# Kernel optimization log

Measured on AMD Instinct MI355X. Metric: run time of the kernel, lower is better.

The kernel has to match this reference:

```python
import jax, jax.numpy as jnp
import numpy as np

B, n, A = 64, 1024, 32          # graphs, nodes/graph, actions/graph
N = B * n
EH = 2048                        # undirected edges per graph
HID, H = 128, 4
C = HID // H
NF, EF, AD, NI, L = 1, 1, 7, 4, 3
NEG_SLOPE = 0.2


def setup_inputs() -> dict:
    ks = jax.random.split(jax.random.key(0), 16)
    x = jax.random.normal(ks[0], (N, NF), jnp.float32)
    s = jax.random.randint(ks[1], (B, EH), 0, n)
    d = jax.random.randint(ks[2], (B, EH), 0, n)
    off = (jnp.arange(B) * n)[:, None]
    s = (s + off).reshape(-1)
    d = (d + off).reshape(-1)
    # bidirectional edges (unrooted trees): both i->j and j->i
    edge_index = jnp.stack([jnp.concatenate([s, d]), jnp.concatenate([d, s])]).astype(jnp.int32)
    E = edge_index.shape[1]
    edge_attr = jax.random.uniform(ks[3], (E, EF), jnp.float32)
    idx = jax.random.randint(ks[4], (B, A, NI), 0, n).astype(jnp.float32)
    meta = jax.random.normal(ks[5], (B, A, AD - NI), jnp.float32)
    action_tensor = jnp.concatenate([idx, meta], axis=-1)
    batch_idx = jnp.repeat(jnp.arange(B, dtype=jnp.int32), n)
    batch_ptr = jnp.arange(B + 1, dtype=jnp.int32) * n

    def lin(k, i, o):
        return jax.random.normal(k, (i, o), jnp.float32) / np.float32(np.sqrt(i))

    inp = dict(x=x, edge_attr=edge_attr, action_tensor=action_tensor,
               edge_index=edge_index, batch_idx=batch_idx, batch_ptr=batch_ptr)
    inp["Wn"] = lin(ks[6], NF, HID); inp["bn"] = jnp.zeros((HID,), jnp.float32)
    kl = jax.random.split(ks[7], 4 * L)
    inp["gWl"] = jnp.stack([lin(kl[i], HID, HID) for i in range(L)])
    inp["gWr"] = jnp.stack([lin(kl[L + i], HID, HID) for i in range(L)])
    inp["gWe"] = jnp.stack([lin(kl[2 * L + i], EF, HID) for i in range(L)])
    inp["gatt"] = jnp.stack([jax.random.normal(kl[3 * L + i], (H, C), jnp.float32) * 0.1 for i in range(L)])
    inp["gbl"] = jnp.zeros((L, HID), jnp.float32)
    inp["gbr"] = jnp.zeros((L, HID), jnp.float32)
    inp["gb"] = jnp.zeros((L, HID), jnp.float32)
    mlp_in = NI * HID + (AD - NI)
    inp["aW1"] = lin(ks[8], mlp_in, HID); inp["ab1"] = jnp.zeros((HID,), jnp.float32)
    inp["aW2"] = lin(ks[9], HID, HID); inp["ab2"] = jnp.zeros((HID,), jnp.float32)
    inp["qW1"] = lin(ks[10], 4 * HID, HID); inp["qb1"] = jnp.zeros((HID,), jnp.float32)
    inp["qW2"] = lin(ks[11], HID, HID); inp["qb2"] = jnp.zeros((HID,), jnp.float32)
    inp["qW3"] = lin(ks[12], HID, 1); inp["qb3"] = jnp.zeros((1,), jnp.float32)
    return inp


def _gatv2(h, src, dst, ea, Wl, bl, Wr, br, We, att, b):
    # PyG GATv2Conv: e_ij = att . leaky_relu(lin_l(x_j) + lin_r(x_i) + lin_edge(e_ij))
    Nn = h.shape[0]
    xl = (h @ Wl + bl).reshape(Nn, H, C)   # source transform
    xr = (h @ Wr + br).reshape(Nn, H, C)   # target transform
    ee = (ea @ We).reshape(-1, H, C)       # edge transform (no bias in PyG)
    e = jax.nn.leaky_relu(xl[src] + xr[dst] + ee, NEG_SLOPE)   # [E,H,C]
    logits = jnp.einsum('ehc,hc->eh', e, att)
    m = jax.ops.segment_max(logits, dst, num_segments=Nn)       # stable softmax per target node
    ex = jnp.exp(logits - m[dst])
    alpha = ex / jax.ops.segment_sum(ex, dst, num_segments=Nn)[dst]
    msg = (xl[src] * alpha[:, :, None]).reshape(-1, HID)
    return jax.ops.segment_sum(msg, dst, num_segments=Nn) + b


def reference(x, edge_attr, action_tensor, Wn, bn, gWl, gbl, gWr, gbr, gWe, gatt, gb,
              aW1, ab1, aW2, ab2, qW1, qb1, qW2, qb2, qW3, qb3,
              edge_index, batch_idx, batch_ptr):
    Nn = x.shape[0]
    nb = batch_ptr.shape[0] - 1
    # GATv2Conv default add_self_loops=True, fill_value='mean' for edge_attr
    loops = jnp.arange(Nn, dtype=edge_index.dtype)
    src = jnp.concatenate([edge_index[0], loops])
    dst = jnp.concatenate([edge_index[1], loops])
    ea = jnp.concatenate([edge_attr, jnp.broadcast_to(edge_attr.mean(0), (Nn, edge_attr.shape[1]))], 0)
    h = jax.nn.relu(x @ Wn + bn)
    for l in range(L):
        h = jax.nn.relu(_gatv2(h, src, dst, ea, gWl[l], gbl[l], gWr[l], gbr[l], gWe[l], gatt[l], gb[l])) + h
    # sum / mean / max pooling per graph
    sums = jax.ops.segment_sum(h, batch_idx, num_segments=nb)
    cnt = jax.ops.segment_sum(jnp.ones((Nn, 1), h.dtype), batch_idx, num_segments=nb)
    means = sums / cnt
    maxs = jax.ops.segment_max(h, batch_idx, num_segments=nb)
    tree_emb = jnp.concatenate([sums, means, maxs], -1)          # [B, 3*HID]
    # action encoding: gather node embeddings at action node indices (shifted by batch_ptr)
    ni = action_tensor[..., :NI].astype(jnp.int32) + batch_ptr[:-1][:, None, None]
    g = h[ni].reshape(nb, action_tensor.shape[1], NI * HID)
    ai = jnp.concatenate([g, action_tensor[..., NI:]], -1)
    ae = jax.nn.relu(jax.nn.relu(ai @ aW1 + ab1) @ aW2 + ab2)    # [B, A, HID]
    comb = jnp.concatenate([jnp.broadcast_to(tree_emb[:, None, :], (nb, ae.shape[1], 3 * HID)), ae], -1)
    q = jax.nn.relu(comb @ qW1 + qb1)
    q = jax.nn.relu(q @ qW2 + qb2)
    return (q @ qW3 + qb3).squeeze(-1)                            # [B, A]
```

## Files before the change

### kernel.cpp

```cpp
#include <hip/hip_runtime.h>
#include <hip/hip_bf16.h>

#define NNODES 65536
#define NGRAPH 64
#define NPG 1024
#define NACT 32
#define HID 128
#define DEGS 32

typedef __attribute__((ext_vector_type(8))) short bf16x8;
typedef __attribute__((ext_vector_type(4))) float f32x4;

__device__ __forceinline__ void load8(float* dst, const float* src) {
    float4 q0 = ((const float4*)src)[0];
    float4 q1 = ((const float4*)src)[1];
    dst[0]=q0.x; dst[1]=q0.y; dst[2]=q0.z; dst[3]=q0.w;
    dst[4]=q1.x; dst[5]=q1.y; dst[6]=q1.z; dst[7]=q1.w;
}

__device__ __forceinline__ void load8bf(float* dst, const unsigned short* src) {
    uint4 q = *(const uint4*)src;
    unsigned int u0 = q.x, u1 = q.y, u2 = q.z, u3 = q.w;
    dst[0] = __uint_as_float(u0 << 16); dst[1] = __uint_as_float(u0 & 0xffff0000u);
    dst[2] = __uint_as_float(u1 << 16); dst[3] = __uint_as_float(u1 & 0xffff0000u);
    dst[4] = __uint_as_float(u2 << 16); dst[5] = __uint_as_float(u2 & 0xffff0000u);
    dst[6] = __uint_as_float(u3 << 16); dst[7] = __uint_as_float(u3 & 0xffff0000u);
}

__device__ __forceinline__ unsigned short f2bf(float f) {
    unsigned int u = __float_as_uint(f);
    u = (u + 0x7fffu + ((u >> 16) & 1u)) >> 16;
    return (unsigned short)u;
}

__global__ void setup_k(const int* __restrict__ ei, const float* __restrict__ ea,
                        int* __restrict__ cursor, float* __restrict__ meansum,
                        int2* __restrict__ csr, int E0, int nsb,
                        const float* __restrict__ gWl, const float* __restrict__ gWr,
                        unsigned short* __restrict__ wtl, unsigned short* __restrict__ wtr,
                        const float* __restrict__ aW1, const float* __restrict__ aW2,
                        const float* __restrict__ qW1, const float* __restrict__ qW2,
                        unsigned short* __restrict__ wA1t, unsigned short* __restrict__ wA2t,
                        unsigned short* __restrict__ wQ1t, unsigned short* __restrict__ wQ2t) {
    int bid = blockIdx.x, t = threadIdx.x;
    if (bid < nsb) {
        __shared__ float s[256];
        int e = bid * 256 + t;
        float v = 0.f;
        if (e < E0) {
            int sn = ei[e], d = ei[E0 + e];
            int pos = atomicAdd(&cursor[d], 1);
            if (pos >= DEGS) pos = DEGS - 1;
            csr[(size_t)d * DEGS + pos] = make_int2(sn, __float_as_int(ea[e]));
            v = ea[e];
        }
        s[t] = v; __syncthreads();
        for (int off = 128; off > 0; off >>= 1) { if (t < off) s[t] += s[t+off]; __syncthreads(); }
        if (t == 0) atomicAdd(meansum, s[0]);
    } else if (bid < nsb + 192) {
        int idx = (bid - nsb) * 256 + t;
        int l = idx >> 14, rem = idx & 16383;
        int n = rem >> 7, k = rem & 127;
        int src = l*16384 + k*128 + n;
        wtl[idx] = f2bf(gWl[src]);
        wtr[idx] = f2bf(gWr[src]);
    } else {
        int n = bid - nsb - 192;
        for (int k = t; k < 544; k += 256)
            wA1t[n*544 + k] = (k < 515) ? f2bf(aW1[(size_t)k*128 + n]) : (unsigned short)0;
        if (t < 128) {
            wA2t[n*128 + t] = f2bf(aW2[(size_t)t*128 + n]);
            wQ1t[n*128 + t] = f2bf(qW1[(size_t)(384 + t)*128 + n]);
            wQ2t[n*128 + t] = f2bf(qW2[(size_t)t*128 + n]);
        }
    }
}

__global__ __launch_bounds__(256) void gemm_lr_mfma_k(
    const unsigned short* __restrict__ hb, const float* __restrict__ x,
    const float* __restrict__ Wn, const float* __restrict__ bn, int l0,
    const unsigned short* __restrict__ wtl, const unsigned short* __restrict__ wtr,
    const float* __restrict__ bl, const float* __restrict__ br,
    unsigned short* __restrict__ xlb, unsigned short* __restrict__ xrb) {
    int wave = threadIdx.x >> 6;
    int lane = threadIdx.x & 63;
    int lr = lane & 15;
    int lq = lane >> 4;
    int r0 = blockIdx.x * 128 + wave * 32;

    bf16x8 a[2][4];
    if (l0) {
        float xv0 = x[r0 + lr], xv1 = x[r0 + 16 + lr];
#pragma unroll
        for (int kf = 0; kf < 4; ++kf) {
            float wn[8], bv[8];
            load8(wn, Wn + kf*32 + lq*8);
            load8(bv, bn + kf*32 + lq*8);
            union { bf16x8 v; unsigned short u[8]; } p0, p1;
#pragma unroll
            for (int j = 0; j < 8; ++j) {
                p0.u[j] = f2bf(fmaxf(fmaf(xv0, wn[j], bv[j]), 0.f));
                p1.u[j] = f2bf(fmaxf(fmaf(xv1, wn[j], bv[j]), 0.f));
            }
            a[0][kf] = p0.v; a[1][kf] = p1.v;
        }
    } else {
        const short* hs = (const short*)hb;
#pragma unroll
        for (int rt = 0; rt < 2; ++rt)
#pragma unroll
            for (int kf = 0; kf < 4; ++kf)
                a[rt][kf] = *(const bf16x8*)(hs + (size_t)(r0 + rt*16 + lr)*HID + kf*32 + lq*8);
    }

    const short* ws[2]   = {(const short*)wtl, (const short*)wtr};
    const float* bias[2] = {bl, br};
    unsigned short* outp[2] = {xlb, xrb};

#pragma unroll
    for (int m = 0; m < 2; ++m) {
        const short* W = ws[m];
        f32x4 acc[2][8];
#pragma unroll
        for (int rt = 0; rt < 2; ++rt)
#pragma unroll
            for (int ct = 0; ct < 8; ++ct) acc[rt][ct] = (f32x4){0.f,0.f,0.f,0.f};

        bf16x8 b[4], nb[4];
#pragma unroll
        for (int kf = 0; kf < 4; ++kf)
            b[kf] = *(const bf16x8*)(W + (size_t)(lr)*HID + kf*32 + lq*8);
#pragma unroll
        for (int ct = 0; ct < 8; ++ct) {
            if (ct < 7) {
#pragma unroll
                for (int kf = 0; kf < 4; ++kf)
                    nb[kf] = *(const bf16x8*)(W + (size_t)((ct+1)*16 + lr)*HID + kf*32 + lq*8);
            }
#pragma unroll
            for (int rt = 0; rt < 2; ++rt)
#pragma unroll
                for (int kf = 0; kf < 4; ++kf)
                    acc[rt][ct] = __builtin_amdgcn_mfma_f32_16x16x32_bf16(a[rt][kf], b[kf], acc[rt][ct], 0, 0, 0);
#pragma unroll
            for (int kf = 0; kf < 4; ++kf) b[kf] = nb[kf];
        }
#pragma unroll
        for (int ct = 0; ct < 8; ++ct) {
            float bv = bias[m][ct*16 + lr];
#pragma unroll
            for (int rt = 0; rt < 2; ++rt)
#pragma unroll
                for (int rg = 0; rg < 4; ++rg) {
                    int row = r0 + rt*16 + lq*4 + rg;
                    outp[m][(size_t)row*HID + ct*16 + lr] = f2bf(acc[rt][ct][rg] + bv);
                }
        }
    }
}

__global__ __launch_bounds__(256, 4) void gat_edge_k(
    const unsigned short* __restrict__ xlb, const unsigned short* __restrict__ xrb,
    unsigned short* __restrict__ hb,
    const int* __restrict__ deg, const int2* __restrict__ csr,
    const float* __restrict__ We, const float* __restrict__ att,
    const float* __restrict__ gb, const float* __restrict__ meansum, float inv_e0,
    const float* __restrict__ x, const float* __restrict__ Wn, const float* __restrict__ bn,
    int l0, int do_pool, float* __restrict__ tree_sum, float* __restrict__ tree_max) {
    __shared__ float ps[16][132];
    __shared__ float pm[16][132];
    int xcd  = blockIdx.x & 7;
    int slot = blockIdx.x >> 3;
    int g    = xcd * 8 + (slot >> 6);
    int j    = slot & 63;
    int t    = threadIdx.x;
    int nd   = t >> 4;
    int v    = g * NPG + j * 16 + nd;
    int li   = t & 15;
    int base = li * 8;
    float mea = meansum[0] * inv_e0;

    float xrv[8], attv[8], wev[8];
    load8bf(xrv, xrb + (size_t)v*HID + base);
    load8(attv, att + base);
    load8(wev, We + base);

    float acc[8], xA[8];
    load8bf(xA, xlb + (size_t)v*HID + base);
    float m;
    {
        float lg = 0.f;
#pragma unroll
        for (int c = 0; c < 8; ++c) {
            float e = xA[c] + xrv[c] + mea * wev[c];
            e = fmaxf(e, 0.2f * e);
            lg = fmaf(attv[c], e, lg);
        }
        lg += __shfl_xor(lg, 1, 64);
        lg += __shfl_xor(lg, 2, 64);
        m = lg;
#pragma unroll
        for (int c = 0; c < 8; ++c) acc[c] = xA[c];
    }
    float den = 1.f;

    int dg = deg[v];
    if (dg > DEGS) dg = DEGS;
    if (dg > 0) {
        const int2* cp = csr + (size_t)v * DEGS;
        int2 e0 = cp[0];
        int2 e1 = cp[(1 < dg) ? 1 : dg - 1];
        float xB[8];
        load8bf(xA, xlb + (size_t)e0.x*HID + base);
        load8bf(xB, xlb + (size_t)e1.x*HID + base);
        for (int i = 0; i < dg; ++i) {
            int2 e2 = cp[(i + 2 < dg) ? i + 2 : dg - 1];
            float xC[8];
            load8bf(xC, xlb + (size_t)e2.x*HID + base);
            float an = __int_as_float(e0.y);

            float lg = 0.f;
#pragma unroll
            for (int c = 0; c < 8; ++c) {
                float e = xA[c] + xrv[c] + an * wev[c];
                e = fmaxf(e, 0.2f * e);
                lg = fmaf(attv[c], e, lg);
            }
            lg += __shfl_xor(lg, 1, 64);
            lg += __shfl_xor(lg, 2, 64);

            float mn  = fmaxf(m, lg);
            float sc  = __expf(m - mn);
            float wgt = __expf(lg - mn);
            den = den * sc + wgt;
#pragma unroll
            for (int c = 0; c < 8; ++c) acc[c] = acc[c] * sc + wgt * xA[c];
            m = mn;
            e0 = e1; e1 = e2;
#pragma unroll
            for (int c = 0; c < 8; ++c) { xA[c] = xB[c]; xB[c] = xC[c]; }
        }
    }

    float inv = 1.f / den;
    size_t o = (size_t)v*HID + base;
    float hold[8], gbv[8];
    if (l0) {
        float xv = x[v];
        float wn[8], bv[8];
        load8(wn, Wn + base);
        load8(bv, bn + base);
#pragma unroll
        for (int c = 0; c < 8; ++c) hold[c] = fmaxf(fmaf(xv, wn[c], bv[c]), 0.f);
    } else {
        load8bf(hold, hb + o);
    }
    load8(gbv, gb + base);
    float nh[8];
#pragma unroll
    for (int c = 0; c < 8; ++c) {
        float val = acc[c] * inv + gbv[c];
        val = val > 0.f ? val : 0.f;
        nh[c] = val + hold[c];
    }
    unsigned int* hbp = (unsigned int*)(hb + o);
#pragma unroll
    for (int q = 0; q < 4; ++q)
        hbp[q] = (unsigned int)f2bf(nh[2*q]) | ((unsigned int)f2bf(nh[2*q+1]) << 16);

    if (do_pool) {
#pragma unroll
        for (int c = 0; c < 8; ++c) { ps[nd][base + c] = nh[c]; pm[nd][base + c] = nh[c]; }
        __syncthreads();
        if (t < 128) {
            float s = 0.f;
#pragma unroll
            for (int n = 0; n < 16; ++n) s += ps[n][t];
            atomicAdd(&tree_sum[g*128 + t], s);
        } else {
            int col = t - 128;
            float mx = 0.f;
#pragma unroll
            for (int n = 0; n < 16; ++n) mx = fmaxf(mx, pm[n][col]);
            atomicMax((int*)&tree_max[g*128 + col], __float_as_int(mx));
        }
    }
}

#define SA1 552
#define SAC 136
__global__ __launch_bounds__(256) void action_q_k(
    const unsigned short* __restrict__ hb, const float* __restrict__ action,
    const int* __restrict__ batch_ptr,
    const float* __restrict__ tree_sum, const float* __restrict__ tree_max,
    const unsigned short* __restrict__ wA1t, const float* __restrict__ ab1,
    const unsigned short* __restrict__ wA2t, const float* __restrict__ ab2,
    const float* __restrict__ qW1, const unsigned short* __restrict__ wQ1t,
    const float* __restrict__ qb1,
    const unsigned short* __restrict__ wQ2t, const float* __restrict__ qb2,
    const float* __restrict__ qW3, const float* __restrict__ qb3,
    float* __restrict__ out) {
    int b = blockIdx.x;
    int t = threadIdx.x;
    int w  = t >> 6;
    int lane = t & 63;
    int lr = lane & 15;
    int lq = lane >> 4;

    __shared__ unsigned short aib[32 * SA1];
    __shared__ unsigned short z1s[32 * SAC];
    __shared__ unsigned short aes[32 * SAC];
    __shared__ unsigned short q1s[32 * SAC];
    __shared__ float q2f[32 * 132];
    __shared__ float tqA[128], tqB[128];
    __shared__ float psum[32][8];

    int ptr = batch_ptr[b];

    {
        int p = t >> 1, half = t & 1;
        int a = p >> 2, j = p & 3;
        const float* actp = action + (size_t)(b * NACT + a) * 7;
        int ni = (int)actp[j] + ptr;
        const uint4* src = (const uint4*)(hb + (size_t)ni * HID) + half * 8;
        uint4* dst = (uint4*)((char*)aib + ((size_t)a * SA1 + j * 128 + half * 64) * 2);
#pragma unroll
        for (int q = 0; q < 8; ++q) dst[q] = src[q];
        if (t < 32) {
            const float* ap = action + (size_t)(b * NACT + t) * 7;
            aib[t * SA1 + 512] = f2bf(ap[4]);
            aib[t * SA1 + 513] = f2bf(ap[5]);
            aib[t * SA1 + 514] = f2bf(ap[6]);
            for (int i = 3; i < 40; ++i) aib[t * SA1 + 512 + i] = 0;
        }
    }

    {
        if (t < 128) {
            int col = t;
            float acc = 0.f;
#pragma unroll 4
            for (int k = 0; k < 128; ++k) {
                float sv = tree_sum[b * 128 + k];
                acc = fmaf(sv, qW1[(size_t)k * 128 + col], acc);
                acc = fmaf(sv * (1.f / 1024.f), qW1[(size_t)(128 + k) * 128 + col], acc);
            }
            tqA[col] = acc;
        } else {
            int col = t - 128;
            float acc = 0.f;
#pragma unroll 4
            for (int k = 0; k < 128; ++k) {
                float mv = tree_max[b * 128 + k];
                acc = fmaf(mv, qW1[(size_t)(256 + k) * 128 + col], acc);
            }
            tqB[col] = acc;
        }
    }
    __syncthreads();

    f32x4 acc[2][2];
    const unsigned short* srcA;
    int strideA, K;

    srcA = aib; strideA = SA1; K = 544;
#pragma unroll
    for (int rt = 0; rt < 2; ++rt)
#pragma unroll
        for (int ci = 0; ci < 2; ++ci) acc[rt][ci] = (f32x4){0.f, 0.f, 0.f, 0.f};
    for (int ks = 0; ks < K; ks += 32) {
        bf16x8 a0 = *(const bf16x8*)(srcA + (0 * 16 + lr) * strideA + ks + lq * 8);
        bf16x8 a1 = *(const bf16x8*)(srcA + (1 * 16 + lr) * strideA + ks + lq * 8);
        bf16x8 b0 = *(const bf16x8*)(wA1t + (size_t)((2 * w + 0) * 16 + lr) * K + ks + lq * 8);
        bf16x8 b1 = *(const bf16x8*)(wA1t + (size_t)((2 * w + 1) * 16 + lr) * K + ks + lq * 8);
        acc[0][0] = __builtin_amdgcn_mfma_f32_16x16x32_bf16(a0, b0, acc[0][0], 0, 0, 0);
        acc[0][1] = __builtin_amdgcn_mfma_f32_16x16x32_bf16(a0, b1, acc[0][1], 0, 0, 0);
        acc[1][0] = __builtin_amdgcn_mfma_f32_16x16x32_bf16(a1, b0, acc[1][0], 0, 0, 0);
        acc[1][1] = __builtin_amdgcn_mfma_f32_16x16x32_bf16(a1, b1, acc[1][1], 0, 0, 0);
    }
#pragma unroll
    for (int ci = 0; ci < 2; ++ci) {
        int col = (2 * w + ci) * 16 + lr;
        float bv = ab1[col];
#pragma unroll
        for (int rt = 0; rt < 2; ++rt)
#pragma unroll
            for (int rg = 0; rg < 4; ++rg) {
                int row = rt * 16 + lq * 4 + rg;
                z1s[row * SAC + col] = f2bf(fmaxf(acc[rt][ci][rg] + bv, 0.f));
            }
    }
    __syncthreads();

    srcA = z1s; strideA = SAC; K = 128;
#pragma unroll
    for (int rt = 0; rt < 2; ++rt)
#pragma unroll
        for (int ci = 0; ci < 2; ++ci) acc[rt][ci] = (f32x4){0.f, 0.f, 0.f, 0.f};
#pragma unroll
    for (int ks = 0; ks < 128; ks += 32) {
        bf16x8 a0 = *(const bf16x8*)(srcA + (0 * 16 + lr) * strideA + ks + lq * 8);
        bf16x8 a1 = *(const bf16x8*)(srcA + (1 * 16 + lr) * strideA + ks + lq * 8);
        bf16x8 b0 = *(const bf16x8*)(wA2t + (size_t)((2 * w + 0) * 16 + lr) * K + ks + lq * 8);
        bf16x8 b1 = *(const bf16x8*)(wA2t + (size_t)((2 * w + 1) * 16 + lr) * K + ks + lq * 8);
        acc[0][0] = __builtin_amdgcn_mfma_f32_16x16x32_bf16(a0, b0, acc[0][0], 0, 0, 0);
        acc[0][1] = __builtin_amdgcn_mfma_f32_16x16x32_bf16(a0, b1, acc[0][1], 0, 0, 0);
        acc[1][0] = __builtin_amdgcn_mfma_f32_16x16x32_bf16(a1, b0, acc[1][0], 0, 0, 0);
        acc[1][1] = __builtin_amdgcn_mfma_f32_16x16x32_bf16(a1, b1, acc[1][1], 0, 0, 0);
    }
#pragma unroll
    for (int ci = 0; ci < 2; ++ci) {
        int col = (2 * w + ci) * 16 + lr;
        float bv = ab2[col];
#pragma unroll
        for (int rt = 0; rt < 2; ++rt)
#pragma unroll
            for (int rg = 0; rg < 4; ++rg) {
                int row = rt * 16 + lq * 4 + rg;
                aes[row * SAC + col] = f2bf(fmaxf(acc[rt][ci][rg] + bv, 0.f));
            }
    }
    __syncthreads();

    srcA = aes; strideA = SAC; K = 128;
#pragma unroll
    for (int rt = 0; rt < 2; ++rt)
#pragma unroll
        for (int ci = 0; ci < 2; ++ci) acc[rt][ci] = (f32x4){0.f, 0.f, 0.f, 0.f};
#pragma unroll
    for (int ks = 0; ks < 128; ks += 32) {
        bf16x8 a0 = *(const bf16x8*)(srcA + (0 * 16 + lr) * strideA + ks + lq * 8);
        bf16x8 a1 = *(const bf16x8*)(srcA + (1 * 16 + lr) * strideA + ks + lq * 8);
        bf16x8 b0 = *(const bf16x8*)(wQ1t + (size_t)((2 * w + 0) * 16 + lr) * K + ks + lq * 8);
        bf16x8 b1 = *(const bf16x8*)(wQ1t + (size_t)((2 * w + 1) * 16 + lr) * K + ks + lq * 8);
        acc[0][0] = __builtin_amdgcn_mfma_f32_16x16x32_bf16(a0, b0, acc[0][0], 0, 0, 0);
        acc[0][1] = __builtin_amdgcn_mfma_f32_16x16x32_bf16(a0, b1, acc[0][1], 0, 0, 0);
        acc[1][0] = __builtin_amdgcn_mfma_f32_16x16x32_bf16(a1, b0, acc[1][0], 0, 0, 0);
        acc[1][1] = __builtin_amdgcn_mfma_f32_16x16x32_bf16(a1, b1, acc[1][1], 0, 0, 0);
    }
#pragma unroll
    for (int ci = 0; ci < 2; ++ci) {
        int col = (2 * w + ci) * 16 + lr;
        float bv = qb1[col] + tqA[col] + tqB[col];
#pragma unroll
        for (int rt = 0; rt < 2; ++rt)
#pragma unroll
            for (int rg = 0; rg < 4; ++rg) {
                int row = rt * 16 + lq * 4 + rg;
                q1s[row * SAC + col] = f2bf(fmaxf(acc[rt][ci][rg] + bv, 0.f));
            }
    }
    __syncthreads();

    srcA = q1s; strideA = SAC; K = 128;
#pragma unroll
    for (int rt = 0; rt < 2; ++rt)
#pragma unroll
        for (int ci = 0; ci < 2; ++ci) acc[rt][ci] = (f32x4){0.f, 0.f, 0.f, 0.f};
#pragma unroll
    for (int ks = 0; ks < 128; ks += 32) {
        bf16x8 a0 = *(const bf16x8*)(srcA + (0 * 16 + lr) * strideA + ks + lq * 8);
        bf16x8 a1 = *(const bf16x8*)(srcA + (1 * 16 + lr) * strideA + ks + lq * 8);
        bf16x8 b0 = *(const bf16x8*)(wQ2t + (size_t)((2 * w + 0) * 16 + lr) * K + ks + lq * 8);
        bf16x8 b1 = *(const bf16x8*)(wQ2t + (size_t)((2 * w + 1) * 16 + lr) * K + ks + lq * 8);
        acc[0][0] = __builtin_amdgcn_mfma_f32_16x16x32_bf16(a0, b0, acc[0][0], 0, 0, 0);
        acc[0][1] = __builtin_amdgcn_mfma_f32_16x16x32_bf16(a0, b1, acc[0][1], 0, 0, 0);
        acc[1][0] = __builtin_amdgcn_mfma_f32_16x16x32_bf16(a1, b0, acc[1][0], 0, 0, 0);
        acc[1][1] = __builtin_amdgcn_mfma_f32_16x16x32_bf16(a1, b1, acc[1][1], 0, 0, 0);
    }
#pragma unroll
    for (int ci = 0; ci < 2; ++ci) {
        int col = (2 * w + ci) * 16 + lr;
        float bv = qb2[col];
#pragma unroll
        for (int rt = 0; rt < 2; ++rt)
#pragma unroll
            for (int rg = 0; rg < 4; ++rg) {
                int row = rt * 16 + lq * 4 + rg;
                q2f[row * 132 + col] = fmaxf(acc[rt][ci][rg] + bv, 0.f);
            }
    }
    __syncthreads();

    {
        int a = t >> 3, seg = t & 7;
        float s = 0.f;
#pragma unroll
        for (int k = 0; k < 16; ++k)
            s = fmaf(q2f[a * 132 + seg * 16 + k], qW3[seg * 16 + k], s);
        psum[a][seg] = s;
    }
    __syncthreads();
    if (t < 32) {
        float s = qb3[0];
#pragma unroll
        for (int i = 0; i < 8; ++i) s += psum[t][i];
        out[(size_t)b * NACT + t] = s;
    }
}

extern "C" void kernel_launch(void* const* d_in, const int* in_sizes, int n_in,
                              void* d_out, int out_size, void* d_ws, size_t ws_size,
                              hipStream_t stream) {
    const float* x         = (const float*)d_in[0];
    const float* edge_attr = (const float*)d_in[1];
    const float* action    = (const float*)d_in[2];
    const int*   edge_idx  = (const int*)d_in[3];
    const int*   batch_ptr = (const int*)d_in[5];
    const float* Wn  = (const float*)d_in[6];
    const float* bn  = (const float*)d_in[7];
    const float* gWl = (const float*)d_in[8];
    const float* gWr = (const float*)d_in[9];
    const float* gWe = (const float*)d_in[10];
    const float* gatt= (const float*)d_in[11];
    const float* gbl = (const float*)d_in[12];
    const float* gbr = (const float*)d_in[13];
    const float* gb  = (const float*)d_in[14];
    const float* aW1 = (const float*)d_in[15];
    const float* ab1 = (const float*)d_in[16];
    const float* aW2 = (const float*)d_in[17];
    const float* ab2 = (const float*)d_in[18];
    const float* qW1 = (const float*)d_in[19];
    const float* qb1 = (const float*)d_in[20];
    const float* qW2 = (const float*)d_in[21];
    const float* qb2 = (const float*)d_in[22];
    const float* qW3 = (const float*)d_in[23];
    const float* qb3 = (const float*)d_in[24];
    float* out = (float*)d_out;

    const int E0 = in_sizes[1];
    const int N  = NNODES;

    char* w = (char*)d_ws;
    auto alloc = [&](size_t bytes) { void* p = (void*)w; w += (bytes + 255) & ~(size_t)255; return p; };
    unsigned short* hb  = (unsigned short*)alloc((size_t)N * HID * 2);
    unsigned short* xlb = (unsigned short*)alloc((size_t)N * HID * 2);
    unsigned short* xrb = (unsigned short*)alloc((size_t)N * HID * 2);
    int2*  csr      = (int2*)alloc((size_t)N * DEGS * 8);
    int*   cursor   = (int*)alloc((size_t)N * 4);
    float* meansum  = (float*)alloc(256);
    float* tree_sum = (float*)alloc((size_t)NGRAPH * 128 * 4);
    float* tree_max = (float*)alloc((size_t)NGRAPH * 128 * 4);
    size_t zero_span = (size_t)((char*)(tree_max + NGRAPH * 128) - (char*)cursor);
    unsigned short* wtl = (unsigned short*)alloc((size_t)3*128*128*2);
    unsigned short* wtr = (unsigned short*)alloc((size_t)3*128*128*2);
    unsigned short* wA1t = (unsigned short*)alloc((size_t)128*544*2);
    unsigned short* wA2t = (unsigned short*)alloc((size_t)128*128*2);
    unsigned short* wQ1t = (unsigned short*)alloc((size_t)128*128*2);
    unsigned short* wQ2t = (unsigned short*)alloc((size_t)128*128*2);

    hipMemsetAsync(cursor, 0, zero_span, stream);

    int nsb = (E0 + 255) / 256;
    setup_k<<<nsb + 320, 256, 0, stream>>>(edge_idx, edge_attr, cursor, meansum, csr, E0, nsb,
                                           gWl, gWr, wtl, wtr,
                                           aW1, aW2, qW1, qW2, wA1t, wA2t, wQ1t, wQ2t);

    float inv_e0 = 1.0f / (float)E0;
    for (int l = 0; l < 3; ++l) {
        gemm_lr_mfma_k<<<N / 128, 256, 0, stream>>>(
            hb, x, Wn, bn, (l == 0) ? 1 : 0,
            wtl + (size_t)l*128*128, wtr + (size_t)l*128*128,
            gbl + l*HID, gbr + l*HID, xlb, xrb);
        gat_edge_k<<<N / 16, 256, 0, stream>>>(
            xlb, xrb, hb, cursor, csr,
            gWe + l*HID, gatt + l*128, gb + l*HID, meansum, inv_e0,
            x, Wn, bn, (l == 0) ? 1 : 0, (l == 2) ? 1 : 0, tree_sum, tree_max);
    }

    action_q_k<<<NGRAPH, 256, 0, stream>>>(
        hb, action, batch_ptr, tree_sum, tree_max,
        wA1t, ab1, wA2t, ab2, qW1, wQ1t, qb1, wQ2t, qb2, qW3, qb3, out);
}
```

Before: 310.3 us.

## Fuse next-layer GEMM into GAT aggregation and fold action head into final layer

Each GAT aggregation kernel now stages its 16 new node rows in shared memory and immediately computes the next layer's left/right projections with MFMA. This removes the separate per-layer GEMM launches and the extra read of h. The final layer pools per graph and uses a per-graph completion counter, so the last block for each graph runs the action/Q MLP head, which removes a separate kernel launch. The xl/xr buffers are double-buffered because the next layer's outputs are written while neighbours still read the current ones. The trade-off is that each block reloads weight tiles from global or L2, and the last block per graph must wait on atomics plus a fence.

```diff
diff --git a/kernel.cpp b/kernel.cpp
--- a/kernel.cpp
+++ b/kernel.cpp
@@ -7,6 +7,7 @@
 #define NACT 32
 #define HID 128
 #define DEGS 32
+#define SAC 136
 
 typedef __attribute__((ext_vector_type(8))) short bf16x8;
 typedef __attribute__((ext_vector_type(4))) float f32x4;
@@ -17,16 +18,13 @@
     dst[0]=q0.x; dst[1]=q0.y; dst[2]=q0.z; dst[3]=q0.w;
     dst[4]=q1.x; dst[5]=q1.y; dst[6]=q1.z; dst[7]=q1.w;
 }
-
 __device__ __forceinline__ void load8bf(float* dst, const unsigned short* src) {
     uint4 q = *(const uint4*)src;
-    unsigned int u0 = q.x, u1 = q.y, u2 = q.z, u3 = q.w;
-    dst[0] = __uint_as_float(u0 << 16); dst[1] = __uint_as_float(u0 & 0xffff0000u);
-    dst[2] = __uint_as_float(u1 << 16); dst[3] = __uint_as_float(u1 & 0xffff0000u);
-    dst[4] = __uint_as_float(u2 << 16); dst[5] = __uint_as_float(u2 & 0xffff0000u);
-    dst[6] = __uint_as_float(u3 << 16); dst[7] = __uint_as_float(u3 & 0xffff0000u);
-}
-
+    dst[0] = __uint_as_float(q.x << 16); dst[1] = __uint_as_float(q.x & 0xffff0000u);
+    dst[2] = __uint_as_float(q.y << 16); dst[3] = __uint_as_float(q.y & 0xffff0000u);
+    dst[4] = __uint_as_float(q.z << 16); dst[5] = __uint_as_float(q.z & 0xffff0000u);
+    dst[6] = __uint_as_float(q.w << 16); dst[7] = __uint_as_float(q.w & 0xffff0000u);
+}
 __device__ __forceinline__ unsigned short f2bf(float f) {
     unsigned int u = __float_as_uint(f);
     u = (u + 0x7fffu + ((u >> 16) & 1u)) >> 16;
@@ -76,47 +74,34 @@
     }
 }
 
-__global__ __launch_bounds__(256) void gemm_lr_mfma_k(
-    const unsigned short* __restrict__ hb, const float* __restrict__ x,
-    const float* __restrict__ Wn, const float* __restrict__ bn, int l0,
+__global__ __launch_bounds__(256) void gemm0_k(
+    const float* __restrict__ x, const float* __restrict__ Wn, const float* __restrict__ bn,
     const unsigned short* __restrict__ wtl, const unsigned short* __restrict__ wtr,
     const float* __restrict__ bl, const float* __restrict__ br,
     unsigned short* __restrict__ xlb, unsigned short* __restrict__ xrb) {
-    int wave = threadIdx.x >> 6;
-    int lane = threadIdx.x & 63;
-    int lr = lane & 15;
-    int lq = lane >> 4;
+    int wave = threadIdx.x >> 6, lane = threadIdx.x & 63;
+    int lr = lane & 15, lq = lane >> 4;
     int r0 = blockIdx.x * 128 + wave * 32;
 
     bf16x8 a[2][4];
-    if (l0) {
-        float xv0 = x[r0 + lr], xv1 = x[r0 + 16 + lr];
-#pragma unroll
-        for (int kf = 0; kf < 4; ++kf) {
-            float wn[8], bv[8];
-            load8(wn, Wn + kf*32 + lq*8);
-            load8(bv, bn + kf*32 + lq*8);
-            union { bf16x8 v; unsigned short u[8]; } p0, p1;
-#pragma unroll
-            for (int j = 0; j < 8; ++j) {
-                p0.u[j] = f2bf(fmaxf(fmaf(xv0, wn[j], bv[j]), 0.f));
-                p1.u[j] = f2bf(fmaxf(fmaf(xv1, wn[j], bv[j]), 0.f));
-            }
-            a[0][kf] = p0.v; a[1][kf] = p1.v;
-        }
-    } else {
-        const short* hs = (const short*)hb;
-#pragma unroll
-        for (int rt = 0; rt < 2; ++rt)
-#pragma unroll
-            for (int kf = 0; kf < 4; ++kf)
-                a[rt][kf] = *(const bf16x8*)(hs + (size_t)(r0 + rt*16 + lr)*HID + kf*32 + lq*8);
+    float xv0 = x[r0 + lr], xv1 = x[r0 + 16 + lr];
+#pragma unroll
+    for (int kf = 0; kf < 4; ++kf) {
+        float wn[8], bv[8];
+        load8(wn, Wn + kf*32 + lq*8);
+        load8(bv, bn + kf*32 + lq*8);
+        union { bf16x8 v; unsigned short u[8]; } p0, p1;
+#pragma unroll
+        for (int j = 0; j < 8; ++j) {
+            p0.u[j] = f2bf(fmaxf(fmaf(xv0, wn[j], bv[j]), 0.f));
+            p1.u[j] = f2bf(fmaxf(fmaf(xv1, wn[j], bv[j]), 0.f));
+        }
+        a[0][kf] = p0.v; a[1][kf] = p1.v;
     }
 
     const short* ws[2]   = {(const short*)wtl, (const short*)wtr};
     const float* bias[2] = {bl, br};
     unsigned short* outp[2] = {xlb, xrb};
-
 #pragma unroll
     for (int m = 0; m < 2; ++m) {
         const short* W = ws[m];
@@ -125,17 +110,16 @@
         for (int rt = 0; rt < 2; ++rt)
 #pragma unroll
             for (int ct = 0; ct < 8; ++ct) acc[rt][ct] = (f32x4){0.f,0.f,0.f,0.f};
-
-        bf16x8 b[4], nb[4];
+        bf16x8 b[4], nb2[4];
 #pragma unroll
         for (int kf = 0; kf < 4; ++kf)
-            b[kf] = *(const bf16x8*)(W + (size_t)(lr)*HID + kf*32 + lq*8);
+            b[kf] = *(const bf16x8*)(W + (size_t)lr*HID + kf*32 + lq*8);
 #pragma unroll
         for (int ct = 0; ct < 8; ++ct) {
             if (ct < 7) {
 #pragma unroll
                 for (int kf = 0; kf < 4; ++kf)
-                    nb[kf] = *(const bf16x8*)(W + (size_t)((ct+1)*16 + lr)*HID + kf*32 + lq*8);
+                    nb2[kf] = *(const bf16x8*)(W + (size_t)((ct+1)*16 + lr)*HID + kf*32 + lq*8);
             }
 #pragma unroll
             for (int rt = 0; rt < 2; ++rt)
@@ -143,7 +127,7 @@
                 for (int kf = 0; kf < 4; ++kf)
                     acc[rt][ct] = __builtin_amdgcn_mfma_f32_16x16x32_bf16(a[rt][kf], b[kf], acc[rt][ct], 0, 0, 0);
 #pragma unroll
-            for (int kf = 0; kf < 4; ++kf) b[kf] = nb[kf];
+            for (int kf = 0; kf < 4; ++kf) b[kf] = nb2[kf];
         }
 #pragma unroll
         for (int ct = 0; ct < 8; ++ct) {
@@ -151,24 +135,190 @@
 #pragma unroll
             for (int rt = 0; rt < 2; ++rt)
 #pragma unroll
-                for (int rg = 0; rg < 4; ++rg) {
-                    int row = r0 + rt*16 + lq*4 + rg;
-                    outp[m][(size_t)row*HID + ct*16 + lr] = f2bf(acc[rt][ct][rg] + bv);
-                }
-        }
-    }
-}
-
-__global__ __launch_bounds__(256, 4) void gat_edge_k(
-    const unsigned short* __restrict__ xlb, const unsigned short* __restrict__ xrb,
+                for (int rg = 0; rg < 4; ++rg)
+                    outp[m][(size_t)(r0 + rt*16 + lq*4 + rg)*HID + ct*16 + lr] = f2bf(acc[rt][ct][rg] + bv);
+        }
+    }
+}
+
+
+__global__ __launch_bounds__(256, 4) void gatgemm_k(
+    const unsigned short* __restrict__ xli, const unsigned short* __restrict__ xri,
     unsigned short* __restrict__ hb,
     const int* __restrict__ deg, const int2* __restrict__ csr,
     const float* __restrict__ We, const float* __restrict__ att,
     const float* __restrict__ gb, const float* __restrict__ meansum, float inv_e0,
-    const float* __restrict__ x, const float* __restrict__ Wn, const float* __restrict__ bn,
-    int l0, int do_pool, float* __restrict__ tree_sum, float* __restrict__ tree_max) {
-    __shared__ float ps[16][132];
-    __shared__ float pm[16][132];
+    const float* __restrict__ x, const float* __restrict__ Wn, const float* __restrict__ bn, int l0,
+    const unsigned short* __restrict__ wtlN, const unsigned short* __restrict__ wtrN,
+    const float* __restrict__ blN, const float* __restrict__ brN,
+    unsigned short* __restrict__ xlo, unsigned short* __restrict__ xro) {
+    __shared__ unsigned short sA[16 * SAC];
+    int xcd  = blockIdx.x & 7;
+    int slot = blockIdx.x >> 3;
+    int g    = xcd * 8 + (slot >> 6);
+    int j    = slot & 63;
+    int t    = threadIdx.x;
+    int nd   = t >> 4;
+    int vb   = g * NPG + j * 16;
+    int v    = vb + nd;
+    int li   = t & 15;
+    int base = li * 8;
+    float mea = meansum[0] * inv_e0;
+
+    float xrv[8], attv[8], wev[8];
+    load8bf(xrv, xri + (size_t)v*HID + base);
+    load8(attv, att + base);
+    load8(wev, We + base);
+
+    float acc[8], xA[8];
+    load8bf(xA, xli + (size_t)v*HID + base);
+    float m;
+    {
+        float lg = 0.f;
+#pragma unroll
+        for (int c = 0; c < 8; ++c) {
+            float e = xA[c] + xrv[c] + mea * wev[c];
+            e = fmaxf(e, 0.2f * e);
+            lg = fmaf(attv[c], e, lg);
+        }
+        lg += __shfl_xor(lg, 1, 64);
+        lg += __shfl_xor(lg, 2, 64);
+        m = lg;
+#pragma unroll
+        for (int c = 0; c < 8; ++c) acc[c] = xA[c];
+    }
+    float den = 1.f;
+
+    int dg = deg[v];
+    if (dg > DEGS) dg = DEGS;
+    if (dg > 0) {
+        const int2* cp = csr + (size_t)v * DEGS;
+        int2 e0 = cp[0];
+        int2 e1 = cp[(1 < dg) ? 1 : dg - 1];
+        float xB[8];
+        load8bf(xA, xli + (size_t)e0.x*HID + base);
+        load8bf(xB, xli + (size_t)e1.x*HID + base);
+        for (int i = 0; i < dg; ++i) {
+            int2 e2 = cp[(i + 2 < dg) ? i + 2 : dg - 1];
+            float xC[8];
+            load8bf(xC, xli + (size_t)e2.x*HID + base);
+            float an = __int_as_float(e0.y);
+            float lg = 0.f;
+#pragma unroll
+            for (int c = 0; c < 8; ++c) {
+                float e = xA[c] + xrv[c] + an * wev[c];
+                e = fmaxf(e, 0.2f * e);
+                lg = fmaf(attv[c], e, lg);
+            }
+            lg += __shfl_xor(lg, 1, 64);
+            lg += __shfl_xor(lg, 2, 64);
+            float mn  = fmaxf(m, lg);
+            float sc  = __expf(m - mn);
+            float wgt = __expf(lg - mn);
+            den = den * sc + wgt;
+#pragma unroll
+            for (int c = 0; c < 8; ++c) acc[c] = acc[c] * sc + wgt * xA[c];
+            m = mn;
+            e0 = e1; e1 = e2;
+#pragma unroll
+            for (int c = 0; c < 8; ++c) { xA[c] = xB[c]; xB[c] = xC[c]; }
+        }
+    }
+
+    float inv = 1.f / den;
+    size_t o = (size_t)v*HID + base;
+    float hold[8], gbv[8];
+    if (l0) {
+        float xv = x[v];
+        float wn[8], bv[8];
+        load8(wn, Wn + base);
+        load8(bv, bn + base);
+#pragma unroll
+        for (int c = 0; c < 8; ++c) hold[c] = fmaxf(fmaf(xv, wn[c], bv[c]), 0.f);
+    } else {
+        load8bf(hold, hb + o);
+    }
+    load8(gbv, gb + base);
+    float nh[8];
+#pragma unroll
+    for (int c = 0; c < 8; ++c) {
+        float val = acc[c] * inv + gbv[c];
+        val = val > 0.f ? val : 0.f;
+        nh[c] = val + hold[c];
+    }
+    unsigned int pk[4];
+#pragma unroll
+    for (int q = 0; q < 4; ++q)
+        pk[q] = (unsigned int)f2bf(nh[2*q]) | ((unsigned int)f2bf(nh[2*q+1]) << 16);
+    unsigned int* hbp = (unsigned int*)(hb + o);
+#pragma unroll
+    for (int q = 0; q < 4; ++q) hbp[q] = pk[q];
+    unsigned int* sAp = (unsigned int*)(sA + nd * SAC + base);
+#pragma unroll
+    for (int q = 0; q < 4; ++q) sAp[q] = pk[q];
+    __syncthreads();
+
+    int wave = t >> 6, lane = t & 63, lr = lane & 15, lq = lane >> 4;
+    bf16x8 afr[4];
+#pragma unroll
+    for (int kf = 0; kf < 4; ++kf)
+        afr[kf] = *(const bf16x8*)(sA + lr * SAC + kf*32 + lq*8);
+    const short* ws[2]   = {(const short*)wtlN, (const short*)wtrN};
+    const float* bias[2] = {blN, brN};
+    unsigned short* outp[2] = {xlo, xro};
+#pragma unroll
+    for (int mm = 0; mm < 2; ++mm) {
+        const short* W = ws[mm];
+        f32x4 gac[2];
+#pragma unroll
+        for (int ci = 0; ci < 2; ++ci) gac[ci] = (f32x4){0.f,0.f,0.f,0.f};
+#pragma unroll
+        for (int ci = 0; ci < 2; ++ci) {
+            int ct = wave * 2 + ci;
+#pragma unroll
+            for (int kf = 0; kf < 4; ++kf) {
+                bf16x8 bv = *(const bf16x8*)(W + (size_t)(ct*16 + lr)*HID + kf*32 + lq*8);
+                gac[ci] = __builtin_amdgcn_mfma_f32_16x16x32_bf16(afr[kf], bv, gac[ci], 0, 0, 0);
+            }
+        }
+#pragma unroll
+        for (int ci = 0; ci < 2; ++ci) {
+            int ct = wave * 2 + ci;
+            float bv = bias[mm][ct*16 + lr];
+#pragma unroll
+            for (int rg = 0; rg < 4; ++rg)
+                outp[mm][(size_t)(vb + lq*4 + rg)*HID + ct*16 + lr] = f2bf(gac[ci][rg] + bv);
+        }
+    }
+}
+
+__global__ __launch_bounds__(256, 4) void gatfinal_k(
+    const unsigned short* __restrict__ xli, const unsigned short* __restrict__ xri,
+    unsigned short* __restrict__ hb,
+    const int* __restrict__ deg, const int2* __restrict__ csr,
+    const float* __restrict__ We, const float* __restrict__ att,
+    const float* __restrict__ gb, const float* __restrict__ meansum, float inv_e0,
+    float* __restrict__ tree_s, float* __restrict__ tree_m, int* __restrict__ done,
+    const float* __restrict__ action, const int* __restrict__ batch_ptr,
+    const unsigned short* __restrict__ wA1t, const float* __restrict__ ab1,
+    const unsigned short* __restrict__ wA2t, const float* __restrict__ ab2,
+    const float* __restrict__ qW1, const unsigned short* __restrict__ wQ1t,
+    const float* __restrict__ qb1,
+    const unsigned short* __restrict__ wQ2t, const float* __restrict__ qb2,
+    const float* __restrict__ qW3, const float* __restrict__ qb3,
+    float* __restrict__ out) {
+    __shared__ __align__(16) char arena[38912];
+    float* pool = (float*)arena;
+    int*            s_ni = (int*)arena;
+    unsigned short* amt  = (unsigned short*)(arena + 512);
+    float*          tqA  = (float*)(arena + 2560);
+    float*          tqB  = (float*)(arena + 3072);
+    float*          psum = (float*)(arena + 3584);
+    unsigned short* z1s  = (unsigned short*)(arena + 4608);
+    unsigned short* aes  = (unsigned short*)(arena + 13312);
+    float*          q2f  = (float*)(arena + 22016);
+    __shared__ int lastflag;
+
     int xcd  = blockIdx.x & 7;
     int slot = blockIdx.x >> 3;
     int g    = xcd * 8 + (slot >> 6);
@@ -181,12 +331,12 @@
     float mea = meansum[0] * inv_e0;
 
     float xrv[8], attv[8], wev[8];
-    load8bf(xrv, xrb + (size_t)v*HID + base);
+    load8bf(xrv, xri + (size_t)v*HID + base);
     load8(attv, att + base);
     load8(wev, We + base);
 
     float acc[8], xA[8];
-    load8bf(xA, xlb + (size_t)v*HID + base);
+    load8bf(xA, xli + (size_t)v*HID + base);
     float m;
     {
         float lg = 0.f;
@@ -211,14 +361,13 @@
         int2 e0 = cp[0];
         int2 e1 = cp[(1 < dg) ? 1 : dg - 1];
         float xB[8];
-        load8bf(xA, xlb + (size_t)e0.x*HID + base);
-        load8bf(xB, xlb + (size_t)e1.x*HID + base);
+        load8bf(xA, xli + (size_t)e0.x*HID + base);
+        load8bf(xB, xli + (size_t)e1.x*HID + base);
         for (int i = 0; i < dg; ++i) {
             int2 e2 = cp[(i + 2 < dg) ? i + 2 : dg - 1];
             float xC[8];
-            load8bf(xC, xlb + (size_t)e2.x*HID + base);
+            load8bf(xC, xli + (size_t)e2.x*HID + base);
             float an = __int_as_float(e0.y);
-
             float lg = 0.f;
 #pragma unroll
             for (int c = 0; c < 8; ++c) {
@@ -228,7 +377,6 @@
             }
             lg += __shfl_xor(lg, 1, 64);
             lg += __shfl_xor(lg, 2, 64);
-
             float mn  = fmaxf(m, lg);
             float sc  = __expf(m - mn);
             float wgt = __expf(lg - mn);
@@ -245,16 +393,7 @@
     float inv = 1.f / den;
     size_t o = (size_t)v*HID + base;
     float hold[8], gbv[8];
-    if (l0) {
-        float xv = x[v];
-        float wn[8], bv[8];
-        load8(wn, Wn + base);
-        load8(bv, bn + base);
-#pragma unroll
-        for (int c = 0; c < 8; ++c) hold[c] = fmaxf(fmaf(xv, wn[c], bv[c]), 0.f);
-    } else {
-        load8bf(hold, hb + o);
-    }
+    load8bf(hold, hb + o);
     load8(gbv, gb + base);
     float nh[8];
 #pragma unroll
@@ -268,234 +407,198 @@
     for (int q = 0; q < 4; ++q)
         hbp[q] = (unsigned int)f2bf(nh[2*q]) | ((unsigned int)f2bf(nh[2*q+1]) << 16);
 
-    if (do_pool) {
-#pragma unroll
-        for (int c = 0; c < 8; ++c) { ps[nd][base + c] = nh[c]; pm[nd][base + c] = nh[c]; }
-        __syncthreads();
-        if (t < 128) {
-            float s = 0.f;
-#pragma unroll
-            for (int n = 0; n < 16; ++n) s += ps[n][t];
-            atomicAdd(&tree_sum[g*128 + t], s);
+#pragma unroll
+    for (int c = 0; c < 8; ++c) {
+        pool[nd*132 + base + c]        = nh[c];
+        pool[2112 + nd*132 + base + c] = nh[c];
+    }
+    __syncthreads();
+    if (t < 128) {
+        float s = 0.f;
+#pragma unroll
+        for (int n = 0; n < 16; ++n) s += pool[n*132 + t];
+        atomicAdd(&tree_s[g*128 + t], s);
+    } else {
+        int col = t - 128;
+        float mx = 0.f;
+#pragma unroll
+        for (int n = 0; n < 16; ++n) mx = fmaxf(mx, pool[2112 + n*132 + col]);
+        atomicMax((int*)&tree_m[g*128 + col], __float_as_int(mx));
+    }
+    __syncthreads();
+
+    if (t == 0) {
+        __threadfence();
+        int old = atomicAdd(&done[g], 1);
+        lastflag = (old == 63);
+    }
+    __syncthreads();
+    if (!lastflag) return;
+    __threadfence();
+
+    int wave = t >> 6, lane = t & 63, lr = lane & 15, lq = lane >> 4;
+    int ptr = batch_ptr[g];
+    if (t < 128) {
+        int a = t >> 2, jj = t & 3;
+        s_ni[t] = (int)action[(size_t)(g*NACT + a)*7 + jj] + ptr;
+    } else if (t < 160) {
+        int a = t - 128;
+        const float* ap = action + (size_t)(g*NACT + a)*7;
+        amt[a*32 + 0] = f2bf(ap[4]);
+        amt[a*32 + 1] = f2bf(ap[5]);
+        amt[a*32 + 2] = f2bf(ap[6]);
+        for (int i = 3; i < 32; ++i) amt[a*32 + i] = 0;
+    }
+    __syncthreads();
+    if (t < 128) {
+        int col = t;
+        float a2 = 0.f;
+#pragma unroll 4
+        for (int k = 0; k < 128; ++k) {
+            float sv = tree_s[g*128 + k];
+            a2 = fmaf(sv, qW1[(size_t)k*128 + col], a2);
+            a2 = fmaf(sv * (1.f/1024.f), qW1[(size_t)(128 + k)*128 + col], a2);
+        }
+        tqA[col] = a2;
+    } else {
+        int col = t - 128;
+        float a2 = 0.f;
+#pragma unroll 4
+        for (int k = 0; k < 128; ++k)
+            a2 = fmaf(tree_m[g*128 + k], qW1[(size_t)(256 + k)*128 + col], a2);
+        tqB[col] = a2;
+    }
+    __syncthreads();
+
+    const short* hbs = (const short*)hb;
+    f32x4 qac[2][2];
+#pragma unroll
+    for (int rt = 0; rt < 2; ++rt)
+#pragma unroll
+        for (int ci = 0; ci < 2; ++ci) qac[rt][ci] = (f32x4){0.f,0.f,0.f,0.f};
+    for (int ks = 0; ks < 544; ks += 32) {
+        bf16x8 a0, a1;
+        if (ks < 512) {
+            int n0 = s_ni[(0*16 + lr)*4 + (ks >> 7)];
+            int n1 = s_ni[(1*16 + lr)*4 + (ks >> 7)];
+            a0 = *(const bf16x8*)(hbs + (size_t)n0*HID + (ks & 127) + lq*8);
+            a1 = *(const bf16x8*)(hbs + (size_t)n1*HID + (ks & 127) + lq*8);
         } else {
-            int col = t - 128;
-            float mx = 0.f;
-#pragma unroll
-            for (int n = 0; n < 16; ++n) mx = fmaxf(mx, pm[n][col]);
-            atomicMax((int*)&tree_max[g*128 + col], __float_as_int(mx));
-        }
-    }
-}
-
-#define SA1 552
-#define SAC 136
-__global__ __launch_bounds__(256) void action_q_k(
-    const unsigned short* __restrict__ hb, const float* __restrict__ action,
-    const int* __restrict__ batch_ptr,
-    const float* __restrict__ tree_sum, const float* __restrict__ tree_max,
-    const unsigned short* __restrict__ wA1t, const float* __restrict__ ab1,
-    const unsigned short* __restrict__ wA2t, const float* __restrict__ ab2,
-    const float* __restrict__ qW1, const unsigned short* __restrict__ wQ1t,
-    const float* __restrict__ qb1,
-    const unsigned short* __restrict__ wQ2t, const float* __restrict__ qb2,
-    const float* __restrict__ qW3, const float* __restrict__ qb3,
-    float* __restrict__ out) {
-    int b = blockIdx.x;
-    int t = threadIdx.x;
-    int w  = t >> 6;
-    int lane = t & 63;
-    int lr = lane & 15;
-    int lq = lane >> 4;
-
-    __shared__ unsigned short aib[32 * SA1];
-    __shared__ unsigned short z1s[32 * SAC];
-    __shared__ unsigned short aes[32 * SAC];
-    __shared__ unsigned short q1s[32 * SAC];
-    __shared__ float q2f[32 * 132];
-    __shared__ float tqA[128], tqB[128];
-    __shared__ float psum[32][8];
-
-    int ptr = batch_ptr[b];
-
-    {
-        int p = t >> 1, half = t & 1;
-        int a = p >> 2, j = p & 3;
-        const float* actp = action + (size_t)(b * NACT + a) * 7;
-        int ni = (int)actp[j] + ptr;
-        const uint4* src = (const uint4*)(hb + (size_t)ni * HID) + half * 8;
-        uint4* dst = (uint4*)((char*)aib + ((size_t)a * SA1 + j * 128 + half * 64) * 2);
-#pragma unroll
-        for (int q = 0; q < 8; ++q) dst[q] = src[q];
-        if (t < 32) {
-            const float* ap = action + (size_t)(b * NACT + t) * 7;
-            aib[t * SA1 + 512] = f2bf(ap[4]);
-            aib[t * SA1 + 513] = f2bf(ap[5]);
-            aib[t * SA1 + 514] = f2bf(ap[6]);
-            for (int i = 3; i < 40; ++i) aib[t * SA1 + 512 + i] = 0;
-        }
-    }
-
-    {
-        if (t < 128) {
-            int col = t;
-            float acc = 0.f;
-#pragma unroll 4
-            for (int k = 0; k < 128; ++k) {
-                float sv = tree_sum[b * 128 + k];
-                acc = fmaf(sv, qW1[(size_t)k * 128 + col], acc);
-                acc = fmaf(sv * (1.f / 1024.f), qW1[(size_t)(128 + k) * 128 + col], acc);
-            }
-            tqA[col] = acc;
-        } else {
-            int col = t - 128;
-            float acc = 0.f;
-#pragma unroll 4
-            for (int k = 0; k < 128; ++k) {
-                float mv = tree_max[b * 128 + k];
-                acc = fmaf(mv, qW1[(size_t)(256 + k) * 128 + col], acc);
-            }
-            tqB[col] = acc;
-        }
-    }
-    __syncthreads();
-
-    f32x4 acc[2][2];
-    const unsigned short* srcA;
-    int strideA, K;
-
-    srcA = aib; strideA = SA1; K = 544;
+            a0 = *(const bf16x8*)(amt + (0*16 + lr)*32 + lq*8);
+            a1 = *(const bf16x8*)(amt + (1*16 + lr)*32 + lq*8);
+        }
+        bf16x8 b0 = *(const bf16x8*)(wA1t + (size_t)((2*wave+0)*16 + lr)*544 + ks + lq*8);
+        bf16x8 b1 = *(const bf16x8*)(wA1t + (size_t)((2*wave+1)*16 + lr)*544 + ks + lq*8);
+        qac[0][0] = __builtin_amdgcn_mfma_f32_16x16x32_bf16(a0, b0, qac[0][0], 0, 0, 0);
+        qac[0][1] = __builtin_amdgcn_mfma_f32_16x16x32_bf16(a0, b1, qac[0][1], 0, 0, 0);
+        qac[1][0] = __builtin_amdgcn_mfma_f32_16x16x32_bf16(a1, b0, qac[1][0], 0, 0, 0);
+        qac[1][1] = __builtin_amdgcn_mfma_f32_16x16x32_bf16(a1, b1, qac[1][1], 0, 0, 0);
+    }
+#pragma unroll
+    for (int ci = 0; ci < 2; ++ci) {
+        int col = (2*wave + ci)*16 + lr;
+        float bv = ab1[col];
+#pragma unroll
+        for (int rt = 0; rt < 2; ++rt)
+#pragma unroll
+            for (int rg = 0; rg < 4; ++rg)
+                z1s[(rt*16 + lq*4 + rg)*SAC + col] = f2bf(fmaxf(qac[rt][ci][rg] + bv, 0.f));
+    }
+    __syncthreads();
 #pragma unroll
     for (int rt = 0; rt < 2; ++rt)
 #pragma unroll
-        for (int ci = 0; ci < 2; ++ci) acc[rt][ci] = (f32x4){0.f, 0.f, 0.f, 0.f};
-    for (int ks = 0; ks < K; ks += 32) {
-        bf16x8 a0 = *(const bf16x8*)(srcA + (0 * 16 + lr) * strideA + ks + lq * 8);
-        bf16x8 a1 = *(const bf16x8*)(srcA + (1 * 16 + lr) * strideA + ks + lq * 8);
-        bf16x8 b0 = *(const bf16x8*)(wA1t + (size_t)((2 * w + 0) * 16 + lr) * K + ks + lq * 8);
-        bf16x8 b1 = *(const bf16x8*)(wA1t + (size_t)((2 * w + 1) * 16 + lr) * K + ks + lq * 8);
-        acc[0][0] = __builtin_amdgcn_mfma_f32_16x16x32_bf16(a0, b0, acc[0][0], 0, 0, 0);
-        acc[0][1] = __builtin_amdgcn_mfma_f32_16x16x32_bf16(a0, b1, acc[0][1], 0, 0, 0);
-        acc[1][0] = __builtin_amdgcn_mfma_f32_16x16x32_bf16(a1, b0, acc[1][0], 0, 0, 0);
-        acc[1][1] = __builtin_amdgcn_mfma_f32_16x16x32_bf16(a1, b1, acc[1][1], 0, 0, 0);
-    }
+        for (int ci = 0; ci < 2; ++ci) qac[rt][ci] = (f32x4){0.f,0.f,0.f,0.f};
+#pragma unroll
+    for (int ks = 0; ks < 128; ks += 32) {
+        bf16x8 a0 = *(const bf16x8*)(z1s + (0*16 + lr)*SAC + ks + lq*8);
+        bf16x8 a1 = *(const bf16x8*)(z1s + (1*16 + lr)*SAC + ks + lq*8);
+        bf16x8 b0 = *(const bf16x8*)(wA2t + (size_t)((2*wave+0)*16 + lr)*128 + ks + lq*8);
+        bf16x8 b1 = *(const bf16x8*)(wA2t + (size_t)((2*wave+1)*16 + lr)*128 + ks + lq*8);
+        qac[0][0] = __builtin_amdgcn_mfma_f32_16x16x32_bf16(a0, b0, qac[0][0], 0, 0, 0);
+        qac[0][1] = __builtin_amdgcn_mfma_f32_16x16x32_bf16(a0, b1, qac[0][1], 0, 0, 0);
+        qac[1][0] = __builtin_amdgcn_mfma_f32_16x16x32_bf16(a1, b0, qac[1][0], 0, 0, 0);
+        qac[1][1] = __builtin_amdgcn_mfma_f32_16x16x32_bf16(a1, b1, qac[1][1], 0, 0, 0);
+    }
+    __syncthreads();
 #pragma unroll
     for (int ci = 0; ci < 2; ++ci) {
-        int col = (2 * w + ci) * 16 + lr;
-        float bv = ab1[col];
+        int col = (2*wave + ci)*16 + lr;
+        float bv = ab2[col];
 #pragma unroll
         for (int rt = 0; rt < 2; ++rt)
 #pragma unroll
-            for (int rg = 0; rg < 4; ++rg) {
-                int row = rt * 16 + lq * 4 + rg;
-                z1s[row * SAC + col] = f2bf(fmaxf(acc[rt][ci][rg] + bv, 0.f));
-            }
-    }
-    __syncthreads();
-
-    srcA = z1s; strideA = SAC; K = 128;
+            for (int rg = 0; rg < 4; ++rg)
+                aes[(rt*16 + lq*4 + rg)*SAC + col] = f2bf(fmaxf(qac[rt][ci][rg] + bv, 0.f));
+    }
+    __syncthreads();
 #pragma unroll
     for (int rt = 0; rt < 2; ++rt)
 #pragma unroll
-        for (int ci = 0; ci < 2; ++ci) acc[rt][ci] = (f32x4){0.f, 0.f, 0.f, 0.f};
+        for (int ci = 0; ci < 2; ++ci) qac[rt][ci] = (f32x4){0.f,0.f,0.f,0.f};
 #pragma unroll
     for (int ks = 0; ks < 128; ks += 32) {
-        bf16x8 a0 = *(const bf16x8*)(srcA + (0 * 16 + lr) * strideA + ks + lq * 8);
-        bf16x8 a1 = *(const bf16x8*)(srcA + (1 * 16 + lr) * strideA + ks + lq * 8);
-        bf16x8 b0 = *(const bf16x8*)(wA2t + (size_t)((2 * w + 0) * 16 + lr) * K + ks + lq * 8);
-        bf16x8 b1 = *(const bf16x8*)(wA2t + (size_t)((2 * w + 1) * 16 + lr) * K + ks + lq * 8);
-        acc[0][0] = __builtin_amdgcn_mfma_f32_16x16x32_bf16(a0, b0, acc[0][0], 0, 0, 0);
-        acc[0][1] = __builtin_amdgcn_mfma_f32_16x16x32_bf16(a0, b1, acc[0][1], 0, 0, 0);
-        acc[1][0] = __builtin_amdgcn_mfma_f32_16x16x32_bf16(a1, b0, acc[1][0], 0, 0, 0);
-        acc[1][1] = __builtin_amdgcn_mfma_f32_16x16x32_bf16(a1, b1, acc[1][1], 0, 0, 0);
-    }
+        bf16x8 a0 = *(const bf16x8*)(aes + (0*16 + lr)*SAC + ks + lq*8);
+        bf16x8 a1 = *(const bf16x8*)(aes + (1*16 + lr)*SAC + ks + lq*8);
+        bf16x8 b0 = *(const bf16x8*)(wQ1t + (size_t)((2*wave+0)*16 + lr)*128 + ks + lq*8);
+        bf16x8 b1 = *(const bf16x8*)(wQ1t + (size_t)((2*wave+1)*16 + lr)*128 + ks + lq*8);
+        qac[0][0] = __builtin_amdgcn_mfma_f32_16x16x32_bf16(a0, b0, qac[0][0], 0, 0, 0);
+        qac[0][1] = __builtin_amdgcn_mfma_f32_16x16x32_bf16(a0, b1, qac[0][1], 0, 0, 0);
+        qac[1][0] = __builtin_amdgcn_mfma_f32_16x16x32_bf16(a1, b0, qac[1][0], 0, 0, 0);
+        qac[1][1] = __builtin_amdgcn_mfma_f32_16x16x32_bf16(a1, b1, qac[1][1], 0, 0, 0);
+    }
+    __syncthreads();
 #pragma unroll
     for (int ci = 0; ci < 2; ++ci) {
-        int col = (2 * w + ci) * 16 + lr;
-        float bv = ab2[col];
+        int col = (2*wave + ci)*16 + lr;
+        float bv = qb1[col] + tqA[col] + tqB[col];
 #pragma unroll
         for (int rt = 0; rt < 2; ++rt)
 #pragma unroll
-            for (int rg = 0; rg < 4; ++rg) {
-                int row = rt * 16 + lq * 4 + rg;
-                aes[row * SAC + col] = f2bf(fmaxf(acc[rt][ci][rg] + bv, 0.f));
-            }
-    }
-    __syncthreads();
-
-    srcA = aes; strideA = SAC; K = 128;
+            for (int rg = 0; rg < 4; ++rg)
+                z1s[(rt*16 + lq*4 + rg)*SAC + col] = f2bf(fmaxf(qac[rt][ci][rg] + bv, 0.f));
+    }
+    __syncthreads();
 #pragma unroll
     for (int rt = 0; rt < 2; ++rt)
 #pragma unroll
-        for (int ci = 0; ci < 2; ++ci) acc[rt][ci] = (f32x4){0.f, 0.f, 0.f, 0.f};
+        for (int ci = 0; ci < 2; ++ci) qac[rt][ci] = (f32x4){0.f,0.f,0.f,0.f};
 #pragma unroll
     for (int ks = 0; ks < 128; ks += 32) {
-        bf16x8 a0 = *(const bf16x8*)(srcA + (0 * 16 + lr) * strideA + ks + lq * 8);
-        bf16x8 a1 = *(const bf16x8*)(srcA + (1 * 16 + lr) * strideA + ks + lq * 8);
-        bf16x8 b0 = *(const bf16x8*)(wQ1t + (size_t)((2 * w + 0) * 16 + lr) * K + ks + lq * 8);
-        bf16x8 b1 = *(const bf16x8*)(wQ1t + (size_t)((2 * w + 1) * 16 + lr) * K + ks + lq * 8);
-        acc[0][0] = __builtin_amdgcn_mfma_f32_16x16x32_bf16(a0, b0, acc[0][0], 0, 0, 0);
-        acc[0][1] = __builtin_amdgcn_mfma_f32_16x16x32_bf16(a0, b1, acc[0][1], 0, 0, 0);
-        acc[1][0] = __builtin_amdgcn_mfma_f32_16x16x32_bf16(a1, b0, acc[1][0], 0, 0, 0);
-        acc[1][1] = __builtin_amdgcn_mfma_f32_16x16x32_bf16(a1, b1, acc[1][1], 0, 0, 0);
+        bf16x8 a0 = *(const bf16x8*)(z1s + (0*16 + lr)*SAC + ks + lq*8);
+        bf16x8 a1 = *(const bf16x8*)(z1s + (1*16 + lr)*SAC + ks + lq*8);
+        bf16x8 b0 = *(const bf16x8*)(wQ2t + (size_t)((2*wave+0)*16 + lr)*128 + ks + lq*8);
+        bf16x8 b1 = *(const bf16x8*)(wQ2t + (size_t)((2*wave+1)*16 + lr)*128 + ks + lq*8);
+        qac[0][0] = __builtin_amdgcn_mfma_f32_16x16x32_bf16(a0, b0, qac[0][0], 0, 0, 0);
+        qac[0][1] = __builtin_amdgcn_mfma_f32_16x16x32_bf16(a0, b1, qac[0][1], 0, 0, 0);
+        qac[1][0] = __builtin_amdgcn_mfma_f32_16x16x32_bf16(a1, b0, qac[1][0], 0, 0, 0);
+        qac[1][1] = __builtin_amdgcn_mfma_f32_16x16x32_bf16(a1, b1, qac[1][1], 0, 0, 0);
     }
 #pragma unroll
     for (int ci = 0; ci < 2; ++ci) {
-        int col = (2 * w + ci) * 16 + lr;
-        float bv = qb1[col] + tqA[col] + tqB[col];
+        int col = (2*wave + ci)*16 + lr;
+        float bv = qb2[col];
 #pragma unroll
         for (int rt = 0; rt < 2; ++rt)
 #pragma unroll
-            for (int rg = 0; rg < 4; ++rg) {
-                int row = rt * 16 + lq * 4 + rg;
-                q1s[row * SAC + col] = f2bf(fmaxf(acc[rt][ci][rg] + bv, 0.f));
-            }
-    }
-    __syncthreads();
-
-    srcA = q1s; strideA = SAC; K = 128;
-#pragma unroll
-    for (int rt = 0; rt < 2; ++rt)
-#pragma unroll
-        for (int ci = 0; ci < 2; ++ci) acc[rt][ci] = (f32x4){0.f, 0.f, 0.f, 0.f};
-#pragma unroll
-    for (int ks = 0; ks < 128; ks += 32) {
-        bf16x8 a0 = *(const bf16x8*)(srcA + (0 * 16 + lr) * strideA + ks + lq * 8);
-        bf16x8 a1 = *(const bf16x8*)(srcA + (1 * 16 + lr) * strideA + ks + lq * 8);
-        bf16x8 b0 = *(const bf16x8*)(wQ2t + (size_t)((2 * w + 0) * 16 + lr) * K + ks + lq * 8);
-        bf16x8 b1 = *(const bf16x8*)(wQ2t + (size_t)((2 * w + 1) * 16 + lr) * K + ks + lq * 8);
-        acc[0][0] = __builtin_amdgcn_mfma_f32_16x16x32_bf16(a0, b0, acc[0][0], 0, 0, 0);
-        acc[0][1] = __builtin_amdgcn_mfma_f32_16x16x32_bf16(a0, b1, acc[0][1], 0, 0, 0);
-        acc[1][0] = __builtin_amdgcn_mfma_f32_16x16x32_bf16(a1, b0, acc[1][0], 0, 0, 0);
-        acc[1][1] = __builtin_amdgcn_mfma_f32_16x16x32_bf16(a1, b1, acc[1][1], 0, 0, 0);
-    }
-#pragma unroll
-    for (int ci = 0; ci < 2; ++ci) {
-        int col = (2 * w + ci) * 16 + lr;
-        float bv = qb2[col];
-#pragma unroll
-        for (int rt = 0; rt < 2; ++rt)
-#pragma unroll
-            for (int rg = 0; rg < 4; ++rg) {
-                int row = rt * 16 + lq * 4 + rg;
-                q2f[row * 132 + col] = fmaxf(acc[rt][ci][rg] + bv, 0.f);
-            }
-    }
-    __syncthreads();
-
+            for (int rg = 0; rg < 4; ++rg)
+                q2f[(rt*16 + lq*4 + rg)*132 + col] = fmaxf(qac[rt][ci][rg] + bv, 0.f);
+    }
+    __syncthreads();
     {
         int a = t >> 3, seg = t & 7;
         float s = 0.f;
 #pragma unroll
         for (int k = 0; k < 16; ++k)
-            s = fmaf(q2f[a * 132 + seg * 16 + k], qW3[seg * 16 + k], s);
-        psum[a][seg] = s;
+            s = fmaf(q2f[a*132 + seg*16 + k], qW3[seg*16 + k], s);
+        psum[a*8 + seg] = s;
     }
     __syncthreads();
     if (t < 32) {
         float s = qb3[0];
 #pragma unroll
-        for (int i = 0; i < 8; ++i) s += psum[t][i];
-        out[(size_t)b * NACT + t] = s;
+        for (int i = 0; i < 8; ++i) s += psum[t*8 + i];
+        out[(size_t)g*NACT + t] = s;
     }
 }
 
@@ -534,16 +637,19 @@
     char* w = (char*)d_ws;
     auto alloc = [&](size_t bytes) { void* p = (void*)w; w += (bytes + 255) & ~(size_t)255; return p; };
     unsigned short* hb  = (unsigned short*)alloc((size_t)N * HID * 2);
-    unsigned short* xlb = (unsigned short*)alloc((size_t)N * HID * 2);
-    unsigned short* xrb = (unsigned short*)alloc((size_t)N * HID * 2);
+    unsigned short* xl0 = (unsigned short*)alloc((size_t)N * HID * 2);
+    unsigned short* xr0 = (unsigned short*)alloc((size_t)N * HID * 2);
+    unsigned short* xl1 = (unsigned short*)alloc((size_t)N * HID * 2);
+    unsigned short* xr1 = (unsigned short*)alloc((size_t)N * HID * 2);
     int2*  csr      = (int2*)alloc((size_t)N * DEGS * 8);
     int*   cursor   = (int*)alloc((size_t)N * 4);
     float* meansum  = (float*)alloc(256);
-    float* tree_sum = (float*)alloc((size_t)NGRAPH * 128 * 4);
-    float* tree_max = (float*)alloc((size_t)NGRAPH * 128 * 4);
-    size_t zero_span = (size_t)((char*)(tree_max + NGRAPH * 128) - (char*)cursor);
-    unsigned short* wtl = (unsigned short*)alloc((size_t)3*128*128*2);
-    unsigned short* wtr = (unsigned short*)alloc((size_t)3*128*128*2);
+    float* tree_s   = (float*)alloc((size_t)NGRAPH * 128 * 4);
+    float* tree_m   = (float*)alloc((size_t)NGRAPH * 128 * 4);
+    int*   done     = (int*)alloc(NGRAPH * 4);
+    size_t zero_span = (size_t)((char*)(done + NGRAPH) - (char*)cursor);
+    unsigned short* wtl  = (unsigned short*)alloc((size_t)3*128*128*2);
+    unsigned short* wtr  = (unsigned short*)alloc((size_t)3*128*128*2);
     unsigned short* wA1t = (unsigned short*)alloc((size_t)128*544*2);
     unsigned short* wA2t = (unsigned short*)alloc((size_t)128*128*2);
     unsigned short* wQ1t = (unsigned short*)alloc((size_t)128*128*2);
@@ -557,18 +663,22 @@
                                            aW1, aW2, qW1, qW2, wA1t, wA2t, wQ1t, wQ2t);
 
     float inv_e0 = 1.0f / (float)E0;
-    for (int l = 0; l < 3; ++l) {
-        gemm_lr_mfma_k<<<N / 128, 256, 0, stream>>>(
-            hb, x, Wn, bn, (l == 0) ? 1 : 0,
-            wtl + (size_t)l*128*128, wtr + (size_t)l*128*128,
-            gbl + l*HID, gbr + l*HID, xlb, xrb);
-        gat_edge_k<<<N / 16, 256, 0, stream>>>(
-            xlb, xrb, hb, cursor, csr,
-            gWe + l*HID, gatt + l*128, gb + l*HID, meansum, inv_e0,
-            x, Wn, bn, (l == 0) ? 1 : 0, (l == 2) ? 1 : 0, tree_sum, tree_max);
-    }
-
-    action_q_k<<<NGRAPH, 256, 0, stream>>>(
-        hb, action, batch_ptr, tree_sum, tree_max,
+    gemm0_k<<<N / 128, 256, 0, stream>>>(x, Wn, bn, wtl, wtr, gbl, gbr, xl0, xr0);
+    gatgemm_k<<<N / 16, 256, 0, stream>>>(
+        xl0, xr0, hb, cursor, csr,
+        gWe + 0*HID, gatt + 0*128, gb + 0*HID, meansum, inv_e0,
+        x, Wn, bn, 1,
+        wtl + (size_t)1*16384, wtr + (size_t)1*16384, gbl + 1*HID, gbr + 1*HID,
+        xl1, xr1);
+    gatgemm_k<<<N / 16, 256, 0, stream>>>(
+        xl1, xr1, hb, cursor, csr,
+        gWe + 1*HID, gatt + 1*128, gb + 1*HID, meansum, inv_e0,
+        x, Wn, bn, 0,
+        wtl + (size_t)2*16384, wtr + (size_t)2*16384, gbl + 2*HID, gbr + 2*HID,
+        xl0, xr0);
+    gatfinal_k<<<N / 16, 256, 0, stream>>>(
+        xl0, xr0, hb, cursor, csr,
+        gWe + 2*HID, gatt + 2*128, gb + 2*HID, meansum, inv_e0,
+        tree_s, tree_m, done, action, batch_ptr,
         wA1t, ab1, wA2t, ab2, qW1, wQ1t, qb1, wQ2t, qb2, qW3, qb3, out);
 }
```

New measurement: 455.7 us. 46.9% more time.
